# Kernel tuning notes

Hardware: AMD Instinct MI355X
Metric: run time of the kernel (lower is better)

Reference implementation:

```python
import jax, jax.numpy as jnp
import numpy as np

N = 100_000      # nodes
E = 1_600_000    # edges
F_IN = 4         # num_features
H = 128          # hidden_channels
C = 5            # num_classes
G = 256          # graphs in batch


def setup_inputs() -> dict:
    key = jax.random.key(0)
    ks = jax.random.split(key, 14)
    x = jax.random.normal(ks[0], (N, F_IN), dtype=jnp.float32)
    edge_index = jax.random.randint(ks[1], (2, E), 0, N, dtype=jnp.int64)
    batch = jnp.sort(jax.random.randint(ks[2], (N,), 0, G, dtype=jnp.int64))
    def lin(k, fan_in, fan_out):
        kw, kb = jax.random.split(k)
        s = 1.0 / np.sqrt(fan_in)
        W = jax.random.uniform(kw, (fan_in, fan_out), jnp.float32, -s, s)
        b = jax.random.uniform(kb, (fan_out,), jnp.float32, -s, s)
        return W, b
    W1, b1 = lin(ks[3], F_IN, H)
    W2, b2 = lin(ks[4], H, H)
    W3, b3 = lin(ks[5], H, H)
    W4, b4 = lin(ks[6], H, H)
    Wl, bl = lin(ks[7], H, C)
    return {"x": x, "edge_index": edge_index, "batch": batch,
            "W1": W1, "b1": b1, "W2": W2, "b2": b2,
            "W3": W3, "b3": b3, "W4": W4, "b4": b4,
            "Wl": Wl, "bl": bl}


def reference(x, edge_index, batch, W1, b1, W2, b2, W3, b3, W4, b4, Wl, bl):
    n = x.shape[0]
    loop = jnp.arange(n, dtype=edge_index.dtype)
    src = jnp.concatenate([edge_index[0], loop])  # [E+N], with self-loops
    dst = jnp.concatenate([edge_index[1], loop])
    # symmetric normalization on A + I (PyG GCNConv default)
    deg = jax.ops.segment_sum(jnp.ones_like(dst, dtype=x.dtype), dst, num_segments=n)
    dinv = deg ** -0.5  # deg >= 1 thanks to self-loops
    coef = dinv[src] * dinv[dst]  # per-edge norm [E+N]

    def conv(h, W, b):
        h = h @ W                               # [N, H]
        msg = h[src] * coef[:, None]            # gather + scale [E+N, H]
        return jax.ops.segment_sum(msg, dst, num_segments=n) + b

    h = jax.nn.relu(conv(x, W1, b1))
    h = jax.nn.relu(conv(h, W2, b2))
    h = jax.nn.relu(conv(h, W3, b3))
    h = jax.nn.relu(conv(h, W4, b4))

    # global_mean_pool over graph ids
    counts = jax.ops.segment_sum(jnp.ones((n,), h.dtype), batch, num_segments=G)
    pooled = jax.ops.segment_sum(h, batch, num_segments=G)
    pooled = pooled / jnp.maximum(counts, 1.0)[:, None]  # [G, H]

    return jax.nn.sigmoid(pooled @ Wl + bl)  # [G, C]
```

## Files before the change

### kernel.cpp

```cpp
#include <hip/hip_runtime.h>
#include <hip/hip_fp8.h>
#include <math.h>

#define N_NODES 100000
#define N_EDGES 1600000
#define F_IN    4
#define HID     128
#define N_CLS   5
#define N_GRAPH 256
#define POOL_SEG 8

#define BSHIFT   9
#define BSIZE    512
#define NBUK     196
#define NCHUNK   200
#define CHUNK    8000
#define BUKCAP   9216

typedef _Float16 f16;
typedef _Float16 f16x2 __attribute__((ext_vector_type(2)));
typedef _Float16 f16x8 __attribute__((ext_vector_type(8)));
typedef float f32x4 __attribute__((ext_vector_type(4)));

__device__ __forceinline__ float rec_coef(unsigned r) {
    return (float)__builtin_bit_cast(_Float16, (unsigned short)(r & 0x7FFFu));
}

__device__ __forceinline__ f16x2 rec_coef2(unsigned r) {
    unsigned c = r & 0x7FFFu;
    return __builtin_bit_cast(f16x2, (c << 16) | c);
}

__device__ __forceinline__ float2 fp8x2_to_f32x2(unsigned short raw) {
    __hip_fp8x2_e4m3 t;
    t.__x = raw;
    return static_cast<float2>(t);
}

#if __has_builtin(__builtin_amdgcn_cvt_pk_f16_fp8)
__device__ __forceinline__ f16x2 cvt_h2(unsigned v) {
    auto t = __builtin_amdgcn_cvt_pk_f16_fp8((short)v);
    return __builtin_bit_cast(f16x2, t);
}
#else
__device__ __forceinline__ f16x2 cvt_h2(unsigned v) {
    float2 f = fp8x2_to_f32x2((unsigned short)v);
    auto t = __builtin_amdgcn_cvt_pkrtz(f.x, f.y);
    return __builtin_bit_cast(f16x2, t);
}
#endif

__device__ __forceinline__ void fma8h(f16x2 c2, uint2 v, f16x2* acc) {
    acc[0] += c2 * cvt_h2(v.x);
    acc[1] += c2 * cvt_h2(v.x >> 16);
    acc[2] += c2 * cvt_h2(v.y);
    acc[3] += c2 * cvt_h2(v.y >> 16);
}

__device__ __forceinline__ f16x2 shfl_xor_h2(f16x2 a, int m) {
    return __builtin_bit_cast(f16x2, __shfl_xor(__builtin_bit_cast(int, a), m, 64));
}


__global__ __launch_bounds__(256) void k_scatterA(const int* __restrict__ src, const int* __restrict__ dst,
                                                  int* __restrict__ gcur, unsigned* __restrict__ bkt) {
    __shared__ int cnt[NBUK];
    __shared__ int cur[NBUK];
    int t = threadIdx.x;
    if (t < NBUK) cnt[t] = 0;
    __syncthreads();
    int base = blockIdx.x * CHUNK;
#pragma unroll
    for (int it = 0; it < 32; ++it) {
        int idx = it * 256 + t;
        if (idx < CHUNK) atomicAdd(&cnt[dst[base + idx] >> BSHIFT], 1);
    }
    __syncthreads();
    if (t < NBUK) cur[t] = atomicAdd(&gcur[t], cnt[t]);
    __syncthreads();
#pragma unroll
    for (int it = 0; it < 32; ++it) {
        int idx = it * 256 + t;
        if (idx < CHUNK) {
            int s = src[base + idx], d = dst[base + idx];
            int b = d >> BSHIFT;
            int p = atomicAdd(&cur[b], 1);
            bkt[p] = ((unsigned)s << BSHIFT) | (unsigned)(d & (BSIZE - 1));
        }
    }
}

__global__ __launch_bounds__(256) void k_hist2(const unsigned* __restrict__ bkt,
                                               const int* __restrict__ gcur,
                                               int* __restrict__ deg, float* __restrict__ dinv,
                                               int* __restrict__ padTot) {
    __shared__ int hist[BSIZE];
    __shared__ int tot;
    int t = threadIdx.x, b = blockIdx.x;
    hist[t] = 0; hist[t + 256] = 0;
    if (t == 0) tot = 0;
    __syncthreads();
    int s0 = b * BUKCAP, s1 = gcur[b];
    for (int e = s0 + t; e < s1; e += 256) atomicAdd(&hist[bkt[e] & (BSIZE - 1)], 1);
    __syncthreads();
    int loc = 0;
#pragma unroll
    for (int h = 0; h < 2; ++h) {
        int l = t + h * 256;
        int node = b * BSIZE + l;
        int d = hist[l];
        if (node < N_NODES) {
            deg[node] = d;
            dinv[node] = rsqrtf((float)d + 1.0f);
        }
        loc += (d + 7) >> 3;
    }
    atomicAdd(&tot, loc);
    __syncthreads();
    if (t == 0) padTot[b] = tot << 3;
}

__global__ __launch_bounds__(256) void k_pscan(const int* __restrict__ padTot, int* __restrict__ padBase,
                                               int* __restrict__ rowptrP) {
    __shared__ int s[256];
    int b = threadIdx.x;
    int v = (b < NBUK) ? padTot[b] : 0;
    s[b] = v;
    __syncthreads();
    for (int off = 1; off < 256; off <<= 1) {
        int u = (b >= off) ? s[b - off] : 0;
        __syncthreads();
        s[b] += u;
        __syncthreads();
    }
    if (b < NBUK) padBase[b] = s[b] - v;
    if (b == 0) {
        padBase[NBUK] = s[NBUK - 1];
        rowptrP[N_NODES] = s[NBUK - 1];
    }
}

__global__ __launch_bounds__(256) void k_local2(const unsigned* __restrict__ bkt,
                                                const int* __restrict__ gcur,
                                                const int* __restrict__ deg,
                                                const float* __restrict__ dinv,
                                                const int* __restrict__ padBase,
                                                int* __restrict__ rowptrP,
                                                unsigned* __restrict__ edges) {
    __shared__ int sc[BSIZE];
    __shared__ int cur[BSIZE];
    __shared__ int st[BSIZE];
    __shared__ float dv[BSIZE];
    int t = threadIdx.x, b = blockIdx.x;
    int base = padBase[b];
    int n0 = b * BSIZE + t, n1 = n0 + 256;
    int d0 = (n0 < N_NODES) ? deg[n0] : 0;
    int d1 = (n1 < N_NODES) ? deg[n1] : 0;
    int p0 = ((d0 + 7) >> 3) << 3;
    int p1 = ((d1 + 7) >> 3) << 3;
    sc[t] = p0; sc[t + 256] = p1;
    dv[t] = (n0 < N_NODES) ? dinv[n0] : 0.f;
    dv[t + 256] = (n1 < N_NODES) ? dinv[n1] : 0.f;
    __syncthreads();
    for (int off = 1; off < BSIZE; off <<= 1) {
        int i0 = t, i1 = t + 256;
        int v0 = (i0 >= off) ? sc[i0 - off] : 0;
        int v1 = (i1 >= off) ? sc[i1 - off] : 0;
        __syncthreads();
        sc[i0] += v0; sc[i1] += v1;
        __syncthreads();
    }
    int off0 = base + sc[t] - p0;
    int off1 = base + sc[t + 256] - p1;
    if (n0 < N_NODES) rowptrP[n0] = off0;
    if (n1 < N_NODES) rowptrP[n1] = off1;
    cur[t] = off0; cur[t + 256] = off1;
    st[t]  = off0; st[t + 256]  = off1;
    int padT = sc[BSIZE - 1];
    for (int i = base + t; i < base + padT; i += 256) edges[i] = 0;
    __syncthreads();
    int s0 = b * BUKCAP, s1 = gcur[b];
    for (int e = s0 + t; e < s1; e += 256) {
        unsigned r = bkt[e];
        int dl = (int)(r & (BSIZE - 1));
        int s = (int)(r >> BSHIFT);
        int p = atomicAdd(&cur[dl], 1);
        int rs = st[dl];
        int sl = p - rs;
        int phys = rs + (sl & ~7) + (((sl & 1) << 2) | ((sl >> 1) & 3));
        float c = dv[dl] * dinv[s];
        unsigned short cb = __builtin_bit_cast(unsigned short, (f16)c);
        edges[phys] = ((unsigned)s << 15) | (unsigned)(cb & 0x7FFFu);
    }
}

__global__ __launch_bounds__(256) void k_aggx1(const float4* __restrict__ x,
                                               const int* __restrict__ rowptrP,
                                               const unsigned* __restrict__ edges,
                                               const float* __restrict__ dinv,
                                               const float* __restrict__ W1, const float* __restrict__ b1,
                                               unsigned* __restrict__ hA) {
    __shared__ float4 sxa[16];
    __shared__ float sW[4 * HID];
    __shared__ float sb[HID];
    int t = threadIdx.x;
    sW[t] = W1[t];
    sW[t + 256] = W1[t + 256];
    if (t < HID) sb[t] = b1[t];
    int grp = t >> 4;
    int l = t & 15;
    int node = blockIdx.x * 16 + grp;
    int beg = rowptrP[node], end = rowptrP[node + 1];
    float ax = 0.f, ay = 0.f, az = 0.f, aw = 0.f;
    for (int e = beg + l; e < end; e += 16) {
        unsigned r = edges[e];
        float c = rec_coef(r);
        float4 v = x[r >> 15];
        ax = fmaf(c, v.x, ax); ay = fmaf(c, v.y, ay);
        az = fmaf(c, v.z, az); aw = fmaf(c, v.w, aw);
    }
#pragma unroll
    for (int off = 1; off < 16; off <<= 1) {
        ax += __shfl_xor(ax, off, 64);
        ay += __shfl_xor(ay, off, 64);
        az += __shfl_xor(az, off, 64);
        aw += __shfl_xor(aw, off, 64);
    }
    if (l == 0) {
        float di = dinv[node];
        float c0 = di * di;
        float4 xv = x[node];
        sxa[grp] = make_float4(fmaf(c0, xv.x, ax), fmaf(c0, xv.y, ay),
                               fmaf(c0, xv.z, az), fmaf(c0, xv.w, aw));
    }
    __syncthreads();

    int node0 = blockIdx.x * 16;
#pragma unroll
    for (int it = 0; it < 2; ++it) {
        int id = it * 256 + t;
        int n = id >> 5;
        int g = id & 31;
        float4 a = sxa[n];
        float c[4];
#pragma unroll
        for (int j = 0; j < 4; ++j) {
            int col = g * 4 + j;
            float v = sb[col];
            v = fmaf(a.x, sW[col],           v);
            v = fmaf(a.y, sW[HID + col],     v);
            v = fmaf(a.z, sW[2 * HID + col], v);
            v = fmaf(a.w, sW[3 * HID + col], v);
            c[j] = fmaxf(v, 0.0f);
        }
        unsigned lo = __hip_fp8x2_e4m3(make_float2(c[0], c[1])).__x;
        unsigned hi = __hip_fp8x2_e4m3(make_float2(c[2], c[3])).__x;
        hA[(node0 + n) * 32 + g] = lo | (hi << 16);
    }
}

template <bool FP8OUT>
__global__ __launch_bounds__(512, 8) void k_aggemm8(const unsigned* __restrict__ h8,
                                                    const int* __restrict__ rowptrP,
                                                    const unsigned* __restrict__ edges,
                                                    const float* __restrict__ dinv,
                                                    const f16* __restrict__ Wp,
                                                    const float* __restrict__ bias,
                                                    void* __restrict__ outv) {
    __shared__ f16 S[16 * HID];
    int wave = threadIdx.x >> 6;
    int lane = threadIdx.x & 63;
    int half = lane >> 5;
    int g    = (lane >> 4) & 1;
    int l    = lane & 15;
    int node0 = blockIdx.x * 16;
    int row   = wave * 2 + half;
    int node  = node0 + row;
    int beg = rowptrP[node];
    int end = rowptrP[node + 1];
    const char* hp = (const char*)h8 + l * 8;

    f16x2 acc[4];
    acc[0] = (f16x2){0, 0}; acc[1] = (f16x2){0, 0};
    acc[2] = (f16x2){0, 0}; acc[3] = (f16x2){0, 0};
    {
        float di = dinv[node];
        f16 c0 = (g == 0) ? (f16)(di * di) : (f16)0.f;
        f16x2 c02; c02.x = c0; c02.y = c0;
        uint2 v = *(const uint2*)(hp + ((size_t)node << 7));
        fma8h(c02, v, acc);
    }

    if (beg < end) {
        uint4 R = *(const uint4*)(edges + beg + g * 4);
        uint2 V0 = *(const uint2*)(hp + ((R.x >> 8) & 0xFFFFFF80u));
        uint2 V1 = *(const uint2*)(hp + ((R.y >> 8) & 0xFFFFFF80u));
        uint2 V2 = *(const uint2*)(hp + ((R.z >> 8) & 0xFFFFFF80u));
        uint2 V3 = *(const uint2*)(hp + ((R.w >> 8) & 0xFFFFFF80u));
        int e = beg;
        while (true) {
            int en = e + 8;
            bool more = en < end;
            uint4 Rc = R;
            uint2 W0 = V0, W1 = V1, W2 = V2, W3 = V3;
            if (more) R = *(const uint4*)(edges + en + g * 4);
            fma8h(rec_coef2(Rc.x), W0, acc);
            fma8h(rec_coef2(Rc.y), W1, acc);
            fma8h(rec_coef2(Rc.z), W2, acc);
            fma8h(rec_coef2(Rc.w), W3, acc);
            if (!more) break;
            V0 = *(const uint2*)(hp + ((R.x >> 8) & 0xFFFFFF80u));
            V1 = *(const uint2*)(hp + ((R.y >> 8) & 0xFFFFFF80u));
            V2 = *(const uint2*)(hp + ((R.z >> 8) & 0xFFFFFF80u));
            V3 = *(const uint2*)(hp + ((R.w >> 8) & 0xFFFFFF80u));
            e = en;
        }
    }

#pragma unroll
    for (int j = 0; j < 4; ++j) acc[j] += shfl_xor_h2(acc[j], 16);

    if ((lane & 16) == 0) {
        f16x8 o;
        o[0] = acc[0][0]; o[1] = acc[0][1]; o[2] = acc[1][0]; o[3] = acc[1][1];
        o[4] = acc[2][0]; o[5] = acc[2][1]; o[6] = acc[3][0]; o[7] = acc[3][1];
        int dw = (l * 4) ^ ((row & 7) << 2);
        *(f16x8*)&S[row * HID + dw * 2] = o;
    }
    __syncthreads();

    {
        int t = wave;
        int m = lane & 15;
        int q = lane >> 4;
        f32x4 c4 = (f32x4){0.f, 0.f, 0.f, 0.f};
#pragma unroll
        for (int ks = 0; ks < 4; ++ks) {
            int dw = (ks * 16 + q * 4) ^ ((m & 7) << 2);
            f16x8 a = *(const f16x8*)&S[m * HID + dw * 2];
            f16x8 b = *(const f16x8*)(Wp + ((size_t)(t * 4 + ks) * 64 + lane) * 8);
            c4 = __builtin_amdgcn_mfma_f32_16x16x32_f16(a, b, c4, 0, 0, 0);
        }
        float bb = bias[t * 16 + m];
#pragma unroll
        for (int r = 0; r < 4; ++r) {
            float val = fmaxf(c4[r] + bb, 0.0f);
            int orow = node0 + q * 4 + r;
            if constexpr (FP8OUT) {
                ((__hip_fp8_e4m3*)outv)[(size_t)orow * HID + t * 16 + m] = __hip_fp8_e4m3(val);
            } else {
                ((f16*)outv)[(size_t)orow * HID + t * 16 + m] = (f16)val;
            }
        }
    }
}

__global__ __launch_bounds__(256) void k_packW3(const float* __restrict__ W2, const float* __restrict__ W3,
                                                const float* __restrict__ W4, f16* __restrict__ Wp,
                                                int* __restrict__ gcur) {
    if (blockIdx.x == 0 && threadIdx.x < NBUK) gcur[threadIdx.x] = threadIdx.x * BUKCAP;
    int idx = blockIdx.x * 256 + threadIdx.x;
    int which = idx >> 14;
    int r = idx & 16383;
    const float* W = (which == 0) ? W2 : (which == 1) ? W3 : W4;
    int j  = r & 7;
    int L  = (r >> 3) & 63;
    int ks = (r >> 9) & 3;
    int ct = r >> 11;
    int k = ks * 32 + (L >> 4) * 8 + j;
    int n = ct * 16 + (L & 15);
    Wp[idx] = (f16)W[k * HID + n];
}

__device__ __forceinline__ int lower_bound_batch(const int* __restrict__ batch, int val) {
    int lo = 0, hi = N_NODES;
    while (lo < hi) { int m = (lo + hi) >> 1; if (batch[m] < val) lo = m + 1; else hi = m; }
    return lo;
}

__global__ __launch_bounds__(128) void k_pool1(const f16* __restrict__ h, const int* __restrict__ batch,
                                               float* __restrict__ partials) {
    int g = blockIdx.x / POOL_SEG;
    int s = blockIdx.x % POOL_SEG;
    int f = threadIdx.x;
    int beg = lower_bound_batch(batch, g);
    int end = lower_bound_batch(batch, g + 1);
    int len = end - beg;
    int sb = beg + (int)(((long long)len * s) / POOL_SEG);
    int se = beg + (int)(((long long)len * (s + 1)) / POOL_SEG);
    float acc = 0.0f;
    for (int i = sb; i < se; ++i) acc += (float)h[i * HID + f];
    partials[(size_t)blockIdx.x * HID + f] = acc;
}

__global__ __launch_bounds__(128) void k_pool2h(const float* __restrict__ partials,
                                                const int* __restrict__ batch,
                                                const float* __restrict__ Wl, const float* __restrict__ bl,
                                                float* __restrict__ out) {
    __shared__ float sp[HID];
    int g = blockIdx.x;
    int f = threadIdx.x;
    float acc = 0.0f;
#pragma unroll
    for (int s = 0; s < POOL_SEG; ++s)
        acc += partials[(size_t)(g * POOL_SEG + s) * HID + f];
    int beg = lower_bound_batch(batch, g);
    int end = lower_bound_batch(batch, g + 1);
    sp[f] = acc / fmaxf((float)(end - beg), 1.0f);
    __syncthreads();
    if (f < N_CLS) {
        float v = bl[f];
        for (int k = 0; k < HID; ++k) v = fmaf(sp[k], Wl[k * N_CLS + f], v);
        out[g * N_CLS + f] = 1.0f / (1.0f + expf(-v));
    }
}

extern "C" void kernel_launch(void* const* d_in, const int* in_sizes, int n_in,
                              void* d_out, int out_size, void* d_ws, size_t ws_size,
                              hipStream_t stream) {
    const float* x     = (const float*)d_in[0];
    const int*   ei    = (const int*)d_in[1];
    const int*   batch = (const int*)d_in[2];
    const float* W1 = (const float*)d_in[3];  const float* b1 = (const float*)d_in[4];
    const float* W2 = (const float*)d_in[5];  const float* b2 = (const float*)d_in[6];
    const float* W3 = (const float*)d_in[7];  const float* b3 = (const float*)d_in[8];
    const float* W4 = (const float*)d_in[9];  const float* b4 = (const float*)d_in[10];
    const float* Wl = (const float*)d_in[11]; const float* bl = (const float*)d_in[12];
    float* out = (float*)d_out;

    const size_t EPAD = (size_t)N_EDGES + (size_t)N_NODES * 16;

    char* p = (char*)d_ws;
    auto alloc = [&](size_t bytes) { char* r = p; p += (bytes + 255) & ~(size_t)255; return (void*)r; };
    int*      gcur    = (int*)     alloc((size_t)NBUK * 4);
    int*      padTot  = (int*)     alloc((size_t)NBUK * 4);
    int*      padBase = (int*)     alloc((size_t)(NBUK + 1) * 4);
    unsigned* bkt     = (unsigned*)alloc((size_t)NBUK * BUKCAP * 4);
    int*      deg     = (int*)     alloc((size_t)N_NODES * 4);
    int*      rowptrP = (int*)     alloc((size_t)(N_NODES + 1) * 4);
    float*    dinv    = (float*)   alloc((size_t)N_NODES * 4);
    unsigned* edges   = (unsigned*)alloc(EPAD * 4);
    unsigned* hA      = (unsigned*)alloc((size_t)N_NODES * HID);
    unsigned* hC      = (unsigned*)alloc((size_t)N_NODES * HID);
    f16*      h4      = (f16*)     alloc((size_t)N_NODES * HID * 2);
    float*    parts   = (float*)   alloc((size_t)N_GRAPH * POOL_SEG * HID * 4);
    f16*      Wp      = (f16*)     alloc((size_t)3 * HID * HID * 2);
    f16*      Wp2 = Wp;
    f16*      Wp3 = Wp + HID * HID;
    f16*      Wp4 = Wp + 2 * HID * HID;

    const int* srcv = ei;
    const int* dstv = ei + N_EDGES;

    k_packW3  <<<192, 256, 0, stream>>>(W2, W3, W4, Wp, gcur);
    k_scatterA<<<NCHUNK, 256, 0, stream>>>(srcv, dstv, gcur, bkt);
    k_hist2   <<<NBUK, 256, 0, stream>>>(bkt, gcur, deg, dinv, padTot);
    k_pscan   <<<1, 256, 0, stream>>>(padTot, padBase, rowptrP);
    k_local2  <<<NBUK, 256, 0, stream>>>(bkt, gcur, deg, dinv, padBase, rowptrP, edges);

    k_aggx1<<<N_NODES / 16, 256, 0, stream>>>((const float4*)x, rowptrP, edges, dinv, W1, b1, hA);

    const int fgrid = N_NODES / 16;
    k_aggemm8<true ><<<fgrid, 512, 0, stream>>>(hA, rowptrP, edges, dinv, Wp2, b2, hC);
    k_aggemm8<true ><<<fgrid, 512, 0, stream>>>(hC, rowptrP, edges, dinv, Wp3, b3, hA);
    k_aggemm8<false><<<fgrid, 512, 0, stream>>>(hA, rowptrP, edges, dinv, Wp4, b4, h4);

    k_pool1 <<<N_GRAPH * POOL_SEG, 128, 0, stream>>>(h4, batch, parts);
    k_pool2h<<<N_GRAPH, 128, 0, stream>>>(parts, batch, Wl, bl, out);
}
```

Before: 307.5 us.

## Split CSR build into quarter-buckets with smaller scatter chunks and padded counters

The scatter kernel now uses 800 chunks of 2000 edges instead of 200 of 8000, which gives more blocks to occupy the GPU. It skips the global atomic for empty buckets, and the global bucket counters are spaced 16 ints apart to avoid contention on shared cache lines. The histogram and local-placement kernels now run on quarter-buckets of 128 nodes (784 blocks instead of 196), so each block filters the full bucket for its quarter, and the prefix scan widens to 1024 threads. Padding zeroing moves to a single hipMemsetAsync over the edge array. In exchange, each bucket's entries are read four times.

```diff
diff --git a/kernel.cpp b/kernel.cpp
--- a/kernel.cpp
+++ b/kernel.cpp
@@ -13,8 +13,9 @@
 #define BSHIFT   9
 #define BSIZE    512
 #define NBUK     196
-#define NCHUNK   200
-#define CHUNK    8000
+#define NQB      784
+#define NCHUNK   800
+#define CHUNK    2000
 #define BUKCAP   9216
 
 typedef _Float16 f16;
@@ -71,15 +72,15 @@
     __syncthreads();
     int base = blockIdx.x * CHUNK;
 #pragma unroll
-    for (int it = 0; it < 32; ++it) {
+    for (int it = 0; it < 8; ++it) {
         int idx = it * 256 + t;
         if (idx < CHUNK) atomicAdd(&cnt[dst[base + idx] >> BSHIFT], 1);
     }
     __syncthreads();
-    if (t < NBUK) cur[t] = atomicAdd(&gcur[t], cnt[t]);
-    __syncthreads();
-#pragma unroll
-    for (int it = 0; it < 32; ++it) {
+    if (t < NBUK) cur[t] = cnt[t] ? atomicAdd(&gcur[t * 16], cnt[t]) : 0;
+    __syncthreads();
+#pragma unroll
+    for (int it = 0; it < 8; ++it) {
         int idx = it * 256 + t;
         if (idx < CHUNK) {
             int s = src[base + idx], d = dst[base + idx];
@@ -94,49 +95,49 @@
                                                const int* __restrict__ gcur,
                                                int* __restrict__ deg, float* __restrict__ dinv,
                                                int* __restrict__ padTot) {
-    __shared__ int hist[BSIZE];
+    __shared__ int hist[128];
     __shared__ int tot;
-    int t = threadIdx.x, b = blockIdx.x;
-    hist[t] = 0; hist[t + 256] = 0;
+    int t = threadIdx.x, qb = blockIdx.x;
+    int b = qb >> 2, q = qb & 3;
+    if (t < 128) hist[t] = 0;
     if (t == 0) tot = 0;
     __syncthreads();
-    int s0 = b * BUKCAP, s1 = gcur[b];
-    for (int e = s0 + t; e < s1; e += 256) atomicAdd(&hist[bkt[e] & (BSIZE - 1)], 1);
-    __syncthreads();
-    int loc = 0;
-#pragma unroll
-    for (int h = 0; h < 2; ++h) {
-        int l = t + h * 256;
-        int node = b * BSIZE + l;
-        int d = hist[l];
+    int s0 = b * BUKCAP, s1 = gcur[b * 16];
+    for (int e = s0 + t; e < s1; e += 256) {
+        int dl = (int)(bkt[e] & (BSIZE - 1));
+        if ((dl >> 7) == q) atomicAdd(&hist[dl & 127], 1);
+    }
+    __syncthreads();
+    if (t < 128) {
+        int node = qb * 128 + t;
+        int d = hist[t];
         if (node < N_NODES) {
             deg[node] = d;
             dinv[node] = rsqrtf((float)d + 1.0f);
         }
-        loc += (d + 7) >> 3;
-    }
-    atomicAdd(&tot, loc);
-    __syncthreads();
-    if (t == 0) padTot[b] = tot << 3;
-}
-
-__global__ __launch_bounds__(256) void k_pscan(const int* __restrict__ padTot, int* __restrict__ padBase,
-                                               int* __restrict__ rowptrP) {
-    __shared__ int s[256];
-    int b = threadIdx.x;
-    int v = (b < NBUK) ? padTot[b] : 0;
-    s[b] = v;
-    __syncthreads();
-    for (int off = 1; off < 256; off <<= 1) {
-        int u = (b >= off) ? s[b - off] : 0;
+        atomicAdd(&tot, (d + 7) >> 3);
+    }
+    __syncthreads();
+    if (t == 0) padTot[qb] = tot << 3;
+}
+
+__global__ __launch_bounds__(1024) void k_pscan(const int* __restrict__ padTot, int* __restrict__ padBase,
+                                                int* __restrict__ rowptrP) {
+    __shared__ int s[1024];
+    int t = threadIdx.x;
+    int v = (t < NQB) ? padTot[t] : 0;
+    s[t] = v;
+    __syncthreads();
+    for (int off = 1; off < 1024; off <<= 1) {
+        int u = (t >= off) ? s[t - off] : 0;
         __syncthreads();
-        s[b] += u;
+        s[t] += u;
         __syncthreads();
     }
-    if (b < NBUK) padBase[b] = s[b] - v;
-    if (b == 0) {
-        padBase[NBUK] = s[NBUK - 1];
-        rowptrP[N_NODES] = s[NBUK - 1];
+    if (t < NQB) padBase[t] = s[t] - v;
+    if (t == 0) {
+        padBase[NQB] = s[NQB - 1];
+        rowptrP[N_NODES] = s[NQB - 1];
     }
 }
 
@@ -147,48 +148,48 @@
                                                 const int* __restrict__ padBase,
                                                 int* __restrict__ rowptrP,
                                                 unsigned* __restrict__ edges) {
-    __shared__ int sc[BSIZE];
-    __shared__ int cur[BSIZE];
-    __shared__ int st[BSIZE];
-    __shared__ float dv[BSIZE];
-    int t = threadIdx.x, b = blockIdx.x;
-    int base = padBase[b];
-    int n0 = b * BSIZE + t, n1 = n0 + 256;
-    int d0 = (n0 < N_NODES) ? deg[n0] : 0;
-    int d1 = (n1 < N_NODES) ? deg[n1] : 0;
-    int p0 = ((d0 + 7) >> 3) << 3;
-    int p1 = ((d1 + 7) >> 3) << 3;
-    sc[t] = p0; sc[t + 256] = p1;
-    dv[t] = (n0 < N_NODES) ? dinv[n0] : 0.f;
-    dv[t + 256] = (n1 < N_NODES) ? dinv[n1] : 0.f;
-    __syncthreads();
-    for (int off = 1; off < BSIZE; off <<= 1) {
-        int i0 = t, i1 = t + 256;
-        int v0 = (i0 >= off) ? sc[i0 - off] : 0;
-        int v1 = (i1 >= off) ? sc[i1 - off] : 0;
+    __shared__ int sc[128];
+    __shared__ int cur[128];
+    __shared__ int st[128];
+    __shared__ float dv[128];
+    int t = threadIdx.x, qb = blockIdx.x;
+    int b = qb >> 2, q = qb & 3;
+    int base = padBase[qb];
+    int node = qb * 128 + t;
+    int pd = 0;
+    if (t < 128) {
+        int d = (node < N_NODES) ? deg[node] : 0;
+        pd = ((d + 7) >> 3) << 3;
+        sc[t] = pd;
+        dv[t] = (node < N_NODES) ? dinv[node] : 0.f;
+    }
+    __syncthreads();
+    for (int off = 1; off < 128; off <<= 1) {
+        int v = 0;
+        if (t < 128 && t >= off) v = sc[t - off];
         __syncthreads();
-        sc[i0] += v0; sc[i1] += v1;
+        if (t < 128) sc[t] += v;
         __syncthreads();
     }
-    int off0 = base + sc[t] - p0;
-    int off1 = base + sc[t + 256] - p1;
-    if (n0 < N_NODES) rowptrP[n0] = off0;
-    if (n1 < N_NODES) rowptrP[n1] = off1;
-    cur[t] = off0; cur[t + 256] = off1;
-    st[t]  = off0; st[t + 256]  = off1;
-    int padT = sc[BSIZE - 1];
-    for (int i = base + t; i < base + padT; i += 256) edges[i] = 0;
-    __syncthreads();
-    int s0 = b * BUKCAP, s1 = gcur[b];
+    if (t < 128) {
+        int o = base + sc[t] - pd;
+        if (node < N_NODES) rowptrP[node] = o;
+        cur[t] = o;
+        st[t] = o;
+    }
+    __syncthreads();
+    int s0 = b * BUKCAP, s1 = gcur[b * 16];
     for (int e = s0 + t; e < s1; e += 256) {
         unsigned r = bkt[e];
         int dl = (int)(r & (BSIZE - 1));
+        if ((dl >> 7) != q) continue;
+        int l = dl & 127;
         int s = (int)(r >> BSHIFT);
-        int p = atomicAdd(&cur[dl], 1);
-        int rs = st[dl];
+        int p = atomicAdd(&cur[l], 1);
+        int rs = st[l];
         int sl = p - rs;
         int phys = rs + (sl & ~7) + (((sl & 1) << 2) | ((sl >> 1) & 3));
-        float c = dv[dl] * dinv[s];
+        float c = dv[l] * dinv[s];
         unsigned short cb = __builtin_bit_cast(unsigned short, (f16)c);
         edges[phys] = ((unsigned)s << 15) | (unsigned)(cb & 0x7FFFu);
     }
@@ -358,7 +359,7 @@
 __global__ __launch_bounds__(256) void k_packW3(const float* __restrict__ W2, const float* __restrict__ W3,
                                                 const float* __restrict__ W4, f16* __restrict__ Wp,
                                                 int* __restrict__ gcur) {
-    if (blockIdx.x == 0 && threadIdx.x < NBUK) gcur[threadIdx.x] = threadIdx.x * BUKCAP;
+    if (blockIdx.x == 0 && threadIdx.x < NBUK) gcur[threadIdx.x * 16] = threadIdx.x * BUKCAP;
     int idx = blockIdx.x * 256 + threadIdx.x;
     int which = idx >> 14;
     int r = idx & 16383;
@@ -428,13 +429,13 @@
     const float* Wl = (const float*)d_in[11]; const float* bl = (const float*)d_in[12];
     float* out = (float*)d_out;
 
-    const size_t EPAD = (size_t)N_EDGES + (size_t)N_NODES * 16;
+    const size_t EPAD = (size_t)N_EDGES + (size_t)N_NODES * 8 + 256;
 
     char* p = (char*)d_ws;
     auto alloc = [&](size_t bytes) { char* r = p; p += (bytes + 255) & ~(size_t)255; return (void*)r; };
-    int*      gcur    = (int*)     alloc((size_t)NBUK * 4);
-    int*      padTot  = (int*)     alloc((size_t)NBUK * 4);
-    int*      padBase = (int*)     alloc((size_t)(NBUK + 1) * 4);
+    int*      gcur    = (int*)     alloc((size_t)NBUK * 16 * 4);
+    int*      padTot  = (int*)     alloc((size_t)NQB * 4);
+    int*      padBase = (int*)     alloc((size_t)(NQB + 1) * 4);
     unsigned* bkt     = (unsigned*)alloc((size_t)NBUK * BUKCAP * 4);
     int*      deg     = (int*)     alloc((size_t)N_NODES * 4);
     int*      rowptrP = (int*)     alloc((size_t)(N_NODES + 1) * 4);
@@ -453,10 +454,11 @@
     const int* dstv = ei + N_EDGES;
 
     k_packW3  <<<192, 256, 0, stream>>>(W2, W3, W4, Wp, gcur);
+    hipMemsetAsync(edges, 0, EPAD * 4, stream);
     k_scatterA<<<NCHUNK, 256, 0, stream>>>(srcv, dstv, gcur, bkt);
-    k_hist2   <<<NBUK, 256, 0, stream>>>(bkt, gcur, deg, dinv, padTot);
-    k_pscan   <<<1, 256, 0, stream>>>(padTot, padBase, rowptrP);
-    k_local2  <<<NBUK, 256, 0, stream>>>(bkt, gcur, deg, dinv, padBase, rowptrP, edges);
+    k_hist2   <<<NQB, 256, 0, stream>>>(bkt, gcur, deg, dinv, padTot);
+    k_pscan   <<<1, 1024, 0, stream>>>(padTot, padBase, rowptrP);
+    k_local2  <<<NQB, 256, 0, stream>>>(bkt, gcur, deg, dinv, padBase, rowptrP, edges);
 
     k_aggx1<<<N_NODES / 16, 256, 0, stream>>>((const float4*)x, rowptrP, edges, dinv, W1, b1, hA);
 
```

Result: slower. 330.5 us (+7.5%).
